# Kernel optimization log

Measured on AMD Instinct MI355X. Metric: run time of the kernel, lower is better.

The kernel has to match this reference:

```python
import jax, jax.numpy as jnp
import numpy as np

H = 1024      # hidden_size
M = 64        # matrix_dim = int(sqrt(4096))
R = 2         # rank
LS = 2048     # local_size = budget_size // 2


def setup_inputs() -> dict:
    key = jax.random.key(0)
    ks = jax.random.split(key, 12)
    B, S = 4, 2048
    def lin(k, fan_in, fan_out):
        # stored as [in, out] so forward is x @ W
        return jax.random.normal(k, (fan_in, fan_out), dtype=jnp.float32) / np.sqrt(fan_in)
    return {
        "x": jax.random.normal(ks[0], (B, S, H), dtype=jnp.float32),
        "W_decay": lin(ks[1], H, 1),
        "W_key": lin(ks[2], H, R * M),
        "W_value": lin(ks[3], H, R * M),
        "W_ql": lin(ks[4], H, M),
        "W_qr": lin(ks[5], H, M),
        "W_rec_out": lin(ks[6], M, H),
        "W_up": lin(ks[7], H, LS),
        "W_gate": lin(ks[8], H, LS),
        "W_down": lin(ks[9], LS, H),
        "init_state": jnp.zeros((M, M), dtype=jnp.float32),
    }


def reference(x, W_decay, W_key, W_value, W_ql, W_qr, W_rec_out, W_up, W_gate, W_down, init_state):
    B, S, _ = x.shape
    # Precompute all per-token projections (vectorized over batch & seq)
    decay = jax.nn.sigmoid(x @ W_decay)[..., 0]            # [B,S]
    keys = (x @ W_key).reshape(B, S, R, M)                 # [B,S,R,M]
    values = (x @ W_value).reshape(B, S, R, M)             # [B,S,R,M]
    write = jnp.einsum('bsrm,bsrn->bsmn', keys, values) / float(R)  # [B,S,M,M]
    ql = x @ W_ql                                          # [B,S,M]
    qr = x @ W_qr                                          # [B,S,M]

    def step(state, inp):
        d, w, ql_t, qr_t = inp                             # d:[B], w:[B,M,M], ql/qr:[B,M]
        d3 = d[:, None, None]
        state = d3 * state + (1.0 - d3) * w                # decayed matrix-state update
        read = jnp.einsum('bm,bmn->bn', ql_t, state) * qr_t  # [B,M]
        return state, read

    state0 = jnp.broadcast_to(init_state, (B, M, M))
    # scan over time axis (time-major inputs)
    _, reads = jax.lax.scan(
        step, state0,
        (decay.transpose(1, 0), write.transpose(1, 0, 2, 3),
         ql.transpose(1, 0, 2), qr.transpose(1, 0, 2)))
    reads = reads.transpose(1, 0, 2)                       # [B,S,M]

    recurrent = jax.nn.silu(reads) @ W_rec_out             # [B,S,H]
    local = ((x @ W_up) * jax.nn.silu(x @ W_gate)) @ W_down  # SwiGLU branch
    return recurrent + local
```

## Files before the change

kernel.cpp:

```cpp
#include <hip/hip_runtime.h>
#include <hip/hip_bf16.h>

typedef __bf16 bf16x8 __attribute__((ext_vector_type(8)));
typedef float f32x4 __attribute__((ext_vector_type(4)));

#define BS   8192
#define Hd   1024
#define LSd  2048
#define Md   64

static __device__ __forceinline__ float bfu2f(unsigned short u) {
  return __uint_as_float(((unsigned int)u) << 16);
}
static __device__ __forceinline__ __hip_bfloat16 f2bf(float f) { return __float2bfloat16(f); }


__global__ __launch_bounds__(256) void conv_bf16_kernel(const float* __restrict__ src,
    __hip_bfloat16* __restrict__ dst, int n) {
  int i = (blockIdx.x * 256 + threadIdx.x) * 4;
  if (i + 3 < n) {
    float4 f = *(const float4*)(src + i);
    dst[i + 0] = f2bf(f.x); dst[i + 1] = f2bf(f.y);
    dst[i + 2] = f2bf(f.z); dst[i + 3] = f2bf(f.w);
  }
}

__global__ __launch_bounds__(256) void prep_wcat_kernel(const float* __restrict__ Wd,
    const float* __restrict__ Wk, const float* __restrict__ Wv,
    const float* __restrict__ Wql, const float* __restrict__ Wqr,
    __hip_bfloat16* __restrict__ out) {
  int i = blockIdx.x * 256 + threadIdx.x;
  int n = i >> 10, h = i & 1023;
  float v = 0.f;
  if (n == 0)        v = Wd[h];
  else if (n < 129)  v = Wk[h * 128 + (n - 1)];
  else if (n < 257)  v = Wv[h * 128 + (n - 129)];
  else if (n < 321)  v = Wql[h * 64 + (n - 257)];
  else if (n < 385)  v = Wqr[h * 64 + (n - 321)];
  out[i] = f2bf(v);
}

__global__ __launch_bounds__(256) void transpose_conv_kernel(const float* __restrict__ src,
    __hip_bfloat16* __restrict__ dst, int R, int C, int c_off) {
  __shared__ float tile[32][33];
  int bc = blockIdx.x * 32, br = blockIdx.y * 32;
  int tx = threadIdx.x & 31, ty = threadIdx.x >> 5;
  #pragma unroll
  for (int i = 0; i < 32; i += 8)
    tile[ty + i][tx] = src[(size_t)(br + ty + i) * C + bc + tx];
  __syncthreads();
  #pragma unroll
  for (int i = 0; i < 32; i += 8)
    dst[(size_t)(bc + c_off + ty + i) * R + br + tx] = f2bf(tile[tx][ty + i]);
}


static __device__ __forceinline__ void stage_tile(const __hip_bfloat16* __restrict__ src, int ld,
    __hip_bfloat16* __restrict__ dst, int tid) {
  #pragma unroll
  for (int it = 0; it < 2; ++it) {
    int idx = tid + it * 256;
    int r = idx >> 2, cc = (idx & 3) * 8;
    *(uint4*)(dst + r * 32 + cc) = *(const uint4*)(src + (size_t)r * ld + cc);
  }
}

static __device__ __forceinline__ void mfma_tiles(const __hip_bfloat16* sA, const __hip_bfloat16* sB,
    int wm, int wn, int fr, int qk, f32x4 acc[4][4]) {
  bf16x8 af[4], bg[4];
  #pragma unroll
  for (int i = 0; i < 4; ++i) af[i] = *(const bf16x8*)(sA + (wm + i * 16 + fr) * 32 + qk);
  #pragma unroll
  for (int j = 0; j < 4; ++j) bg[j] = *(const bf16x8*)(sB + (wn + j * 16 + fr) * 32 + qk);
  #pragma unroll
  for (int i = 0; i < 4; ++i)
    #pragma unroll
    for (int j = 0; j < 4; ++j)
      acc[i][j] = __builtin_amdgcn_mfma_f32_16x16x32_bf16(af[i], bg[j], acc[i][j], 0, 0, 0);
}

__global__ __launch_bounds__(256, 2) void gemm_proj_kernel(const __hip_bfloat16* __restrict__ A,
    const __hip_bfloat16* __restrict__ Bt, float* __restrict__ C) {
  __shared__ __align__(16) __hip_bfloat16 sA[128 * 32];
  __shared__ __align__(16) __hip_bfloat16 sB[128 * 32];
  int tid = threadIdx.x, nb = blockIdx.x, mb = blockIdx.y;
  int wave = tid >> 6, lane = tid & 63;
  int wm = (wave >> 1) * 64, wn = (wave & 1) * 64;
  int fr = lane & 15, qk = (lane >> 4) * 8, q4 = (lane >> 4) * 4;
  f32x4 acc[4][4] = {};
  const __hip_bfloat16* Atile = A + (size_t)mb * 128 * Hd;
  const __hip_bfloat16* Btile = Bt + (size_t)nb * 128 * Hd;
  for (int kt = 0; kt < Hd; kt += 32) {
    __syncthreads();
    stage_tile(Atile + kt, Hd, sA, tid);
    stage_tile(Btile + kt, Hd, sB, tid);
    __syncthreads();
    mfma_tiles(sA, sB, wm, wn, fr, qk, acc);
  }
  #pragma unroll
  for (int i = 0; i < 4; ++i)
    #pragma unroll
    for (int j = 0; j < 4; ++j) {
      int row = mb * 128 + wm + i * 16 + q4;
      int col = nb * 128 + wn + j * 16 + fr;
      #pragma unroll
      for (int rg = 0; rg < 4; ++rg)
        C[(size_t)(row + rg) * 512 + col] = acc[i][j][rg];
    }
}

__global__ __launch_bounds__(256, 2) void gemm_upgate_kernel(const __hip_bfloat16* __restrict__ A,
    const __hip_bfloat16* __restrict__ Bt, __hip_bfloat16* __restrict__ hout) {
  __shared__ __align__(16) __hip_bfloat16 sA[128 * 32];
  __shared__ __align__(16) __hip_bfloat16 sBu[128 * 32];
  __shared__ __align__(16) __hip_bfloat16 sBg[128 * 32];
  int tid = threadIdx.x, nb = blockIdx.x, mb = blockIdx.y;
  int wave = tid >> 6, lane = tid & 63;
  int wm = (wave >> 1) * 64, wn = (wave & 1) * 64;
  int fr = lane & 15, qk = (lane >> 4) * 8, q4 = (lane >> 4) * 4;
  f32x4 accu[4][4] = {}, accg[4][4] = {};
  const __hip_bfloat16* Atile = A + (size_t)mb * 128 * Hd;
  const __hip_bfloat16* Bu = Bt + (size_t)(nb * 128) * Hd;
  const __hip_bfloat16* Bg = Bt + (size_t)(2048 + nb * 128) * Hd;
  for (int kt = 0; kt < Hd; kt += 32) {
    __syncthreads();
    stage_tile(Atile + kt, Hd, sA, tid);
    stage_tile(Bu + kt, Hd, sBu, tid);
    stage_tile(Bg + kt, Hd, sBg, tid);
    __syncthreads();
    mfma_tiles(sA, sBu, wm, wn, fr, qk, accu);
    mfma_tiles(sA, sBg, wm, wn, fr, qk, accg);
  }
  #pragma unroll
  for (int i = 0; i < 4; ++i)
    #pragma unroll
    for (int j = 0; j < 4; ++j) {
      int col = nb * 128 + wn + j * 16 + fr;
      #pragma unroll
      for (int rg = 0; rg < 4; ++rg) {
        int row = mb * 128 + wm + i * 16 + q4 + rg;
        float u = accu[i][j][rg], g = accg[i][j][rg];
        float hv = u * g / (1.f + __expf(-g));
        hout[(size_t)row * LSd + col] = f2bf(hv);
      }
    }
}

__global__ __launch_bounds__(256, 2) void gemm_final_kernel(const __hip_bfloat16* __restrict__ A,
    const __hip_bfloat16* __restrict__ Bt, const __hip_bfloat16* __restrict__ A2,
    const __hip_bfloat16* __restrict__ B2t, float* __restrict__ C) {
  __shared__ __align__(16) __hip_bfloat16 sA[128 * 32];
  __shared__ __align__(16) __hip_bfloat16 sB[128 * 32];
  int tid = threadIdx.x, nb = blockIdx.x, mb = blockIdx.y;
  int wave = tid >> 6, lane = tid & 63;
  int wm = (wave >> 1) * 64, wn = (wave & 1) * 64;
  int fr = lane & 15, qk = (lane >> 4) * 8, q4 = (lane >> 4) * 4;
  f32x4 acc[4][4] = {};
  const __hip_bfloat16* Atile = A + (size_t)mb * 128 * LSd;
  const __hip_bfloat16* Btile = Bt + (size_t)nb * 128 * LSd;
  for (int kt = 0; kt < LSd; kt += 32) {
    __syncthreads();
    stage_tile(Atile + kt, LSd, sA, tid);
    stage_tile(Btile + kt, LSd, sB, tid);
    __syncthreads();
    mfma_tiles(sA, sB, wm, wn, fr, qk, acc);
  }
  const __hip_bfloat16* A2t = A2 + (size_t)mb * 128 * Md;
  const __hip_bfloat16* B2tile = B2t + (size_t)nb * 128 * Md;
  for (int kt = 0; kt < Md; kt += 32) {
    __syncthreads();
    stage_tile(A2t + kt, Md, sA, tid);
    stage_tile(B2tile + kt, Md, sB, tid);
    __syncthreads();
    mfma_tiles(sA, sB, wm, wn, fr, qk, acc);
  }
  #pragma unroll
  for (int i = 0; i < 4; ++i)
    #pragma unroll
    for (int j = 0; j < 4; ++j) {
      int row = mb * 128 + wm + i * 16 + q4;
      int col = nb * 128 + wn + j * 16 + fr;
      #pragma unroll
      for (int rg = 0; rg < 4; ++rg)
        C[(size_t)(row + rg) * Hd + col] = acc[i][j][rg];
    }
}


__global__ __launch_bounds__(256) void scan_chunk_kernel(const float* __restrict__ proj,
    float* __restrict__ Lam, float* __restrict__ udv, float* __restrict__ alpha,
    float* __restrict__ dS) {
  int bc = blockIdx.x, t0 = bc * 64, tid = threadIdx.x;
  __shared__ float d_s[64], ld_s[64], Lam_s[64], u_s[64];
  __shared__ __align__(16) __hip_bfloat16 k_s[128 * 64];
  __shared__ __align__(16) __hip_bfloat16 v_s[128 * 64];
  if (tid < 64) {
    float z = proj[(size_t)(t0 + tid) * 512];
    float dd = 1.f / (1.f + __expf(-z));
    float l = (z >= 0.f) ? -log1pf(__expf(-z)) : (z - log1pf(__expf(z)));
    d_s[tid] = dd; ld_s[tid] = l;
  }
  __syncthreads();
  if (tid == 0) {
    float s = 0.f;
    for (int j = 0; j < 64; ++j) { s += ld_s[j]; Lam_s[j] = s; }
  }
  __syncthreads();
  float Lend = Lam_s[63];
  if (tid < 64) {
    u_s[tid] = (1.f - d_s[tid]) * __expf(Lend - Lam_s[tid]) * 0.5f;
    Lam[t0 + tid] = Lam_s[tid];
    udv[t0 + tid] = (1.f - d_s[tid]) * 0.5f;
  }
  if (tid == 0) alpha[bc] = __expf(Lend);
  __syncthreads();
  for (int i = tid; i < 128 * 64; i += 256) {
    int jr = i >> 6, m = i & 63, j = jr >> 1, r = jr & 1;
    const float* rowp = proj + (size_t)(t0 + j) * 512;
    k_s[i] = f2bf(u_s[j] * rowp[1 + r * 64 + m]);
    v_s[i] = f2bf(rowp[129 + r * 64 + m]);
  }
  __syncthreads();
  int m0 = (tid & 15) * 4, n0 = (tid >> 4) * 4;
  float acc[4][4] = {{0.f}};
  for (int jr = 0; jr < 128; ++jr) {
    ushort4 ku = *(const ushort4*)&k_s[jr * 64 + m0];
    ushort4 vu = *(const ushort4*)&v_s[jr * 64 + n0];
    float k0 = bfu2f(ku.x), k1 = bfu2f(ku.y), k2 = bfu2f(ku.z), k3 = bfu2f(ku.w);
    float v0 = bfu2f(vu.x), v1 = bfu2f(vu.y), v2 = bfu2f(vu.z), v3 = bfu2f(vu.w);
    acc[0][0] += k0 * v0; acc[0][1] += k0 * v1; acc[0][2] += k0 * v2; acc[0][3] += k0 * v3;
    acc[1][0] += k1 * v0; acc[1][1] += k1 * v1; acc[1][2] += k1 * v2; acc[1][3] += k1 * v3;
    acc[2][0] += k2 * v0; acc[2][1] += k2 * v1; acc[2][2] += k2 * v2; acc[2][3] += k2 * v3;
    acc[3][0] += k3 * v0; acc[3][1] += k3 * v1; acc[3][2] += k3 * v2; acc[3][3] += k3 * v3;
  }
  float* outp = dS + (size_t)bc * 4096;
  #pragma unroll
  for (int a = 0; a < 4; ++a)
    #pragma unroll
    for (int b2 = 0; b2 < 4; ++b2)
      outp[(m0 + a) * 64 + (n0 + b2)] = acc[a][b2];
}

__global__ __launch_bounds__(256) void scan_cross_kernel(const float* __restrict__ dS,
    const float* __restrict__ alpha, const float* __restrict__ init_state,
    float* __restrict__ Sin) {
  int idx = blockIdx.x * 256 + threadIdx.x;
  int b = idx >> 12, e = idx & 4095;
  float s = init_state[e];
  for (int c = 0; c < 32; ++c) {
    int bc = b * 32 + c;
    Sin[(size_t)bc * 4096 + e] = s;
    s = alpha[bc] * s + dS[(size_t)bc * 4096 + e];
  }
}

#define QLD 68

__global__ __launch_bounds__(256) void scan_read_kernel(const float* __restrict__ proj,
    const float* __restrict__ Lam, const float* __restrict__ udv,
    const float* __restrict__ Sin, __hip_bfloat16* __restrict__ Rd) {
  int bc = blockIdx.x, t0 = bc * 64, tid = threadIdx.x;
  __shared__ __align__(16) __hip_bfloat16 ql_s[64 * QLD];
  __shared__ __align__(16) __hip_bfloat16 kv_s[128 * 64];
  __shared__ __align__(16) __hip_bfloat16 S_s[64 * 64];
  __shared__ __align__(16) __hip_bfloat16 P_s[128 * 64];
  __shared__ float Lam_s[64], ud_s[64], eL_s[64];
  for (int i = tid; i < 64 * 64; i += 256) {
    int t = i >> 6, m = i & 63;
    ql_s[t * QLD + m] = f2bf(proj[(size_t)(t0 + t) * 512 + 257 + m]);
    S_s[i] = f2bf(Sin[(size_t)bc * 4096 + i]);
  }
  for (int i = tid; i < 128 * 64; i += 256) {
    int jr = i >> 6, m = i & 63, j = jr >> 1, r = jr & 1;
    kv_s[i] = f2bf(proj[(size_t)(t0 + j) * 512 + 1 + r * 64 + m]);
  }
  if (tid < 64) {
    float L = Lam[t0 + tid];
    Lam_s[tid] = L; ud_s[tid] = udv[t0 + tid]; eL_s[tid] = __expf(L);
  }
  __syncthreads();
  int tr = (tid & 15) * 4, n0 = (tid >> 4) * 4;
  float acc[4][4] = {{0.f}};
  for (int mb4 = 0; mb4 < 64; mb4 += 4) {
    float sm[4][4];
    #pragma unroll
    for (int mm = 0; mm < 4; ++mm) {
      ushort4 sv = *(const ushort4*)&S_s[(mb4 + mm) * 64 + n0];
      sm[mm][0] = bfu2f(sv.x); sm[mm][1] = bfu2f(sv.y);
      sm[mm][2] = bfu2f(sv.z); sm[mm][3] = bfu2f(sv.w);
    }
    #pragma unroll
    for (int a = 0; a < 4; ++a) {
      ushort4 qa = *(const ushort4*)&ql_s[(tr + a) * QLD + mb4];
      float q0 = bfu2f(qa.x), q1 = bfu2f(qa.y), q2 = bfu2f(qa.z), q3 = bfu2f(qa.w);
      #pragma unroll
      for (int b2 = 0; b2 < 4; ++b2)
        acc[a][b2] += q0 * sm[0][b2] + q1 * sm[1][b2] + q2 * sm[2][b2] + q3 * sm[3][b2];
    }
  }
  #pragma unroll
  for (int a = 0; a < 4; ++a) {
    float e = eL_s[tr + a];
    #pragma unroll
    for (int b2 = 0; b2 < 4; ++b2) acc[a][b2] *= e;
  }
  {
    int jr = tid >> 1, j = jr >> 1, tb = (tid & 1) * 32;
    float dot[32];
    #pragma unroll
    for (int t2 = 0; t2 < 32; ++t2) dot[t2] = 0.f;
    for (int m = 0; m < 64; m += 4) {
      ushort4 kb = *(const ushort4*)&kv_s[jr * 64 + m];
      float k0 = bfu2f(kb.x), k1 = bfu2f(kb.y), k2 = bfu2f(kb.z), k3 = bfu2f(kb.w);
      #pragma unroll
      for (int t2 = 0; t2 < 32; ++t2) {
        ushort4 qa = *(const ushort4*)&ql_s[(tb + t2) * QLD + m];
        dot[t2] += bfu2f(qa.x) * k0 + bfu2f(qa.y) * k1 + bfu2f(qa.z) * k2 + bfu2f(qa.w) * k3;
      }
    }
    #pragma unroll
    for (int t2 = 0; t2 < 32; ++t2) {
      int t = tb + t2;
      float coef = (j <= t) ? ud_s[j] * __expf(Lam_s[t] - Lam_s[j]) : 0.f;
      P_s[jr * 64 + t] = f2bf(dot[t2] * coef);
    }
  }
  __syncthreads();
  for (int i = tid; i < 128 * 64; i += 256) {
    int jr = i >> 6, m = i & 63, j = jr >> 1, r = jr & 1;
    kv_s[i] = f2bf(proj[(size_t)(t0 + j) * 512 + 129 + r * 64 + m]);
  }
  __syncthreads();
  for (int jr = 0; jr < 128; ++jr) {
    ushort4 pu = *(const ushort4*)&P_s[jr * 64 + tr];
    ushort4 vu = *(const ushort4*)&kv_s[jr * 64 + n0];
    float p0 = bfu2f(pu.x), p1 = bfu2f(pu.y), p2 = bfu2f(pu.z), p3 = bfu2f(pu.w);
    float v0 = bfu2f(vu.x), v1 = bfu2f(vu.y), v2 = bfu2f(vu.z), v3 = bfu2f(vu.w);
    acc[0][0] += p0 * v0; acc[0][1] += p0 * v1; acc[0][2] += p0 * v2; acc[0][3] += p0 * v3;
    acc[1][0] += p1 * v0; acc[1][1] += p1 * v1; acc[1][2] += p1 * v2; acc[1][3] += p1 * v3;
    acc[2][0] += p2 * v0; acc[2][1] += p2 * v1; acc[2][2] += p2 * v2; acc[2][3] += p2 * v3;
    acc[3][0] += p3 * v0; acc[3][1] += p3 * v1; acc[3][2] += p3 * v2; acc[3][3] += p3 * v3;
  }
  #pragma unroll
  for (int a = 0; a < 4; ++a) {
    int t = t0 + tr + a;
    const float* qrp = proj + (size_t)t * 512 + 321;
    #pragma unroll
    for (int b2 = 0; b2 < 4; ++b2) {
      float rv = acc[a][b2] * qrp[n0 + b2];
      float sv = rv / (1.f + __expf(-rv));
      Rd[(size_t)t * 64 + n0 + b2] = f2bf(sv);
    }
  }
}


extern "C" void kernel_launch(void* const* d_in, const int* in_sizes, int n_in,
                              void* d_out, int out_size, void* d_ws, size_t ws_size,
                              hipStream_t stream) {
  const float* x      = (const float*)d_in[0];
  const float* W_dec  = (const float*)d_in[1];
  const float* W_key  = (const float*)d_in[2];
  const float* W_val  = (const float*)d_in[3];
  const float* W_ql   = (const float*)d_in[4];
  const float* W_qr   = (const float*)d_in[5];
  const float* W_rec  = (const float*)d_in[6];
  const float* W_up   = (const float*)d_in[7];
  const float* W_gate = (const float*)d_in[8];
  const float* W_down = (const float*)d_in[9];
  const float* init_state = (const float*)d_in[10];
  float* out = (float*)d_out;

  char* w = (char*)d_ws;
  auto take = [&](size_t bytes) { char* p = w; w += (bytes + 255) & ~(size_t)255; return p; };
  __hip_bfloat16* x_bf   = (__hip_bfloat16*)take((size_t)BS * Hd * 2);
  __hip_bfloat16* Wcat_t = (__hip_bfloat16*)take((size_t)512 * Hd * 2);
  __hip_bfloat16* Wug_t  = (__hip_bfloat16*)take((size_t)4096 * Hd * 2);
  __hip_bfloat16* Wdn_t  = (__hip_bfloat16*)take((size_t)Hd * LSd * 2);
  __hip_bfloat16* Wrc_t  = (__hip_bfloat16*)take((size_t)Hd * Md * 2);
  float* proj  = (float*)take((size_t)BS * 512 * 4);
  float* Lam   = (float*)take((size_t)BS * 4);
  float* udv   = (float*)take((size_t)BS * 4);
  float* alpha = (float*)take((size_t)128 * 4);
  float* dS    = (float*)take((size_t)128 * 4096 * 4);
  float* Sin   = (float*)take((size_t)128 * 4096 * 4);
  __hip_bfloat16* Rd   = (__hip_bfloat16*)take((size_t)BS * Md * 2);
  __hip_bfloat16* hbuf = (__hip_bfloat16*)take((size_t)BS * LSd * 2);

  conv_bf16_kernel<<<8192, 256, 0, stream>>>(x, x_bf, BS * Hd);
  prep_wcat_kernel<<<2048, 256, 0, stream>>>(W_dec, W_key, W_val, W_ql, W_qr, Wcat_t);
  transpose_conv_kernel<<<dim3(64, 32), 256, 0, stream>>>(W_up,   Wug_t, Hd, LSd, 0);
  transpose_conv_kernel<<<dim3(64, 32), 256, 0, stream>>>(W_gate, Wug_t, Hd, LSd, 2048);
  transpose_conv_kernel<<<dim3(32, 64), 256, 0, stream>>>(W_down, Wdn_t, LSd, Hd, 0);
  transpose_conv_kernel<<<dim3(32, 2),  256, 0, stream>>>(W_rec,  Wrc_t, Md, Hd, 0);

  gemm_proj_kernel<<<dim3(4, 64), 256, 0, stream>>>(x_bf, Wcat_t, proj);

  scan_chunk_kernel<<<128, 256, 0, stream>>>(proj, Lam, udv, alpha, dS);
  scan_cross_kernel<<<64, 256, 0, stream>>>(dS, alpha, init_state, Sin);
  scan_read_kernel<<<128, 256, 0, stream>>>(proj, Lam, udv, Sin, Rd);

  gemm_upgate_kernel<<<dim3(16, 64), 256, 0, stream>>>(x_bf, Wug_t, hbuf);
  gemm_final_kernel<<<dim3(8, 64), 256, 0, stream>>>(hbuf, Wdn_t, Rd, Wrc_t, out);
}
```

Measured before the change: 338.6 us.

## Stage GEMM tiles with direct global-to-LDS loads in fragment-major layout

```diff
diff --git a/kernel.cpp b/kernel.cpp
--- a/kernel.cpp
+++ b/kernel.cpp
@@ -20,8 +20,12 @@
   int i = (blockIdx.x * 256 + threadIdx.x) * 4;
   if (i + 3 < n) {
     float4 f = *(const float4*)(src + i);
-    dst[i + 0] = f2bf(f.x); dst[i + 1] = f2bf(f.y);
-    dst[i + 2] = f2bf(f.z); dst[i + 3] = f2bf(f.w);
+    ushort4 o;
+    o.x = (unsigned short)(__bfloat16_as_ushort(f2bf(f.x)));
+    o.y = (unsigned short)(__bfloat16_as_ushort(f2bf(f.y)));
+    o.z = (unsigned short)(__bfloat16_as_ushort(f2bf(f.z)));
+    o.w = (unsigned short)(__bfloat16_as_ushort(f2bf(f.w)));
+    *(ushort4*)(dst + i) = o;
   }
 }
 
@@ -55,28 +59,51 @@
 }
 
 
-static __device__ __forceinline__ void stage_tile(const __hip_bfloat16* __restrict__ src, int ld,
-    __hip_bfloat16* __restrict__ dst, int tid) {
+static __device__ __forceinline__ void stage_async(const __hip_bfloat16* __restrict__ src, int ld,
+    __hip_bfloat16* __restrict__ dst, int wave, int lane) {
+  int fr = lane & 15, ch = lane >> 4;
   #pragma unroll
   for (int it = 0; it < 2; ++it) {
-    int idx = tid + it * 256;
-    int r = idx >> 2, cc = (idx & 3) * 8;
-    *(uint4*)(dst + r * 32 + cc) = *(const uint4*)(src + (size_t)r * ld + cc);
-  }
-}
-
-static __device__ __forceinline__ void mfma_tiles(const __hip_bfloat16* sA, const __hip_bfloat16* sB,
-    int wm, int wn, int fr, int qk, f32x4 acc[4][4]) {
+    int ri = wave * 2 + it;
+    int row = ri * 16 + fr;
+    __builtin_amdgcn_global_load_lds(
+        (const __attribute__((address_space(1))) void*)(src + (size_t)row * ld + ch * 8),
+        (__attribute__((address_space(3))) void*)(dst + ri * 512),
+        16, 0, 0);
+  }
+}
+
+static __device__ __forceinline__ void mfma_single(const __hip_bfloat16* sA, const __hip_bfloat16* sB,
+    int wm16, int wn16, int lane, f32x4 acc[4][4]) {
   bf16x8 af[4], bg[4];
   #pragma unroll
-  for (int i = 0; i < 4; ++i) af[i] = *(const bf16x8*)(sA + (wm + i * 16 + fr) * 32 + qk);
-  #pragma unroll
-  for (int j = 0; j < 4; ++j) bg[j] = *(const bf16x8*)(sB + (wn + j * 16 + fr) * 32 + qk);
+  for (int i = 0; i < 4; ++i) af[i] = *(const bf16x8*)(sA + (wm16 + i) * 512 + lane * 8);
+  #pragma unroll
+  for (int j = 0; j < 4; ++j) bg[j] = *(const bf16x8*)(sB + (wn16 + j) * 512 + lane * 8);
   #pragma unroll
   for (int i = 0; i < 4; ++i)
     #pragma unroll
     for (int j = 0; j < 4; ++j)
       acc[i][j] = __builtin_amdgcn_mfma_f32_16x16x32_bf16(af[i], bg[j], acc[i][j], 0, 0, 0);
+}
+
+static __device__ __forceinline__ void mfma_dual(const __hip_bfloat16* sA,
+    const __hip_bfloat16* sBu, const __hip_bfloat16* sBg,
+    int wm16, int wn16, int lane, f32x4 accu[4][4], f32x4 accg[4][4]) {
+  bf16x8 af[4], bu[4], bg[4];
+  #pragma unroll
+  for (int i = 0; i < 4; ++i) af[i] = *(const bf16x8*)(sA + (wm16 + i) * 512 + lane * 8);
+  #pragma unroll
+  for (int j = 0; j < 4; ++j) bu[j] = *(const bf16x8*)(sBu + (wn16 + j) * 512 + lane * 8);
+  #pragma unroll
+  for (int j = 0; j < 4; ++j) bg[j] = *(const bf16x8*)(sBg + (wn16 + j) * 512 + lane * 8);
+  #pragma unroll
+  for (int i = 0; i < 4; ++i)
+    #pragma unroll
+    for (int j = 0; j < 4; ++j) {
+      accu[i][j] = __builtin_amdgcn_mfma_f32_16x16x32_bf16(af[i], bu[j], accu[i][j], 0, 0, 0);
+      accg[i][j] = __builtin_amdgcn_mfma_f32_16x16x32_bf16(af[i], bg[j], accg[i][j], 0, 0, 0);
+    }
 }
 
 __global__ __launch_bounds__(256, 2) void gemm_proj_kernel(const __hip_bfloat16* __restrict__ A,
@@ -85,24 +112,24 @@
   __shared__ __align__(16) __hip_bfloat16 sB[128 * 32];
   int tid = threadIdx.x, nb = blockIdx.x, mb = blockIdx.y;
   int wave = tid >> 6, lane = tid & 63;
-  int wm = (wave >> 1) * 64, wn = (wave & 1) * 64;
-  int fr = lane & 15, qk = (lane >> 4) * 8, q4 = (lane >> 4) * 4;
+  int wm16 = (wave >> 1) * 4, wn16 = (wave & 1) * 4;
+  int fr = lane & 15, q4 = (lane >> 4) * 4;
   f32x4 acc[4][4] = {};
   const __hip_bfloat16* Atile = A + (size_t)mb * 128 * Hd;
   const __hip_bfloat16* Btile = Bt + (size_t)nb * 128 * Hd;
   for (int kt = 0; kt < Hd; kt += 32) {
     __syncthreads();
-    stage_tile(Atile + kt, Hd, sA, tid);
-    stage_tile(Btile + kt, Hd, sB, tid);
-    __syncthreads();
-    mfma_tiles(sA, sB, wm, wn, fr, qk, acc);
+    stage_async(Atile + kt, Hd, sA, wave, lane);
+    stage_async(Btile + kt, Hd, sB, wave, lane);
+    __syncthreads();
+    mfma_single(sA, sB, wm16, wn16, lane, acc);
   }
   #pragma unroll
   for (int i = 0; i < 4; ++i)
     #pragma unroll
     for (int j = 0; j < 4; ++j) {
-      int row = mb * 128 + wm + i * 16 + q4;
-      int col = nb * 128 + wn + j * 16 + fr;
+      int row = mb * 128 + (wm16 + i) * 16 + q4;
+      int col = nb * 128 + (wn16 + j) * 16 + fr;
       #pragma unroll
       for (int rg = 0; rg < 4; ++rg)
         C[(size_t)(row + rg) * 512 + col] = acc[i][j][rg];
@@ -116,29 +143,28 @@
   __shared__ __align__(16) __hip_bfloat16 sBg[128 * 32];
   int tid = threadIdx.x, nb = blockIdx.x, mb = blockIdx.y;
   int wave = tid >> 6, lane = tid & 63;
-  int wm = (wave >> 1) * 64, wn = (wave & 1) * 64;
-  int fr = lane & 15, qk = (lane >> 4) * 8, q4 = (lane >> 4) * 4;
+  int wm16 = (wave >> 1) * 4, wn16 = (wave & 1) * 4;
+  int fr = lane & 15, q4 = (lane >> 4) * 4;
   f32x4 accu[4][4] = {}, accg[4][4] = {};
   const __hip_bfloat16* Atile = A + (size_t)mb * 128 * Hd;
   const __hip_bfloat16* Bu = Bt + (size_t)(nb * 128) * Hd;
   const __hip_bfloat16* Bg = Bt + (size_t)(2048 + nb * 128) * Hd;
   for (int kt = 0; kt < Hd; kt += 32) {
     __syncthreads();
-    stage_tile(Atile + kt, Hd, sA, tid);
-    stage_tile(Bu + kt, Hd, sBu, tid);
-    stage_tile(Bg + kt, Hd, sBg, tid);
-    __syncthreads();
-    mfma_tiles(sA, sBu, wm, wn, fr, qk, accu);
-    mfma_tiles(sA, sBg, wm, wn, fr, qk, accg);
+    stage_async(Atile + kt, Hd, sA, wave, lane);
+    stage_async(Bu + kt, Hd, sBu, wave, lane);
+    stage_async(Bg + kt, Hd, sBg, wave, lane);
+    __syncthreads();
+    mfma_dual(sA, sBu, sBg, wm16, wn16, lane, accu, accg);
   }
   #pragma unroll
   for (int i = 0; i < 4; ++i)
     #pragma unroll
     for (int j = 0; j < 4; ++j) {
-      int col = nb * 128 + wn + j * 16 + fr;
+      int col = nb * 128 + (wn16 + j) * 16 + fr;
       #pragma unroll
       for (int rg = 0; rg < 4; ++rg) {
-        int row = mb * 128 + wm + i * 16 + q4 + rg;
+        int row = mb * 128 + (wm16 + i) * 16 + q4 + rg;
         float u = accu[i][j][rg], g = accg[i][j][rg];
         float hv = u * g / (1.f + __expf(-g));
         hout[(size_t)row * LSd + col] = f2bf(hv);
@@ -153,33 +179,33 @@
   __shared__ __align__(16) __hip_bfloat16 sB[128 * 32];
   int tid = threadIdx.x, nb = blockIdx.x, mb = blockIdx.y;
   int wave = tid >> 6, lane = tid & 63;
-  int wm = (wave >> 1) * 64, wn = (wave & 1) * 64;
-  int fr = lane & 15, qk = (lane >> 4) * 8, q4 = (lane >> 4) * 4;
+  int wm16 = (wave >> 1) * 4, wn16 = (wave & 1) * 4;
+  int fr = lane & 15, q4 = (lane >> 4) * 4;
   f32x4 acc[4][4] = {};
   const __hip_bfloat16* Atile = A + (size_t)mb * 128 * LSd;
   const __hip_bfloat16* Btile = Bt + (size_t)nb * 128 * LSd;
   for (int kt = 0; kt < LSd; kt += 32) {
     __syncthreads();
-    stage_tile(Atile + kt, LSd, sA, tid);
-    stage_tile(Btile + kt, LSd, sB, tid);
-    __syncthreads();
-    mfma_tiles(sA, sB, wm, wn, fr, qk, acc);
+    stage_async(Atile + kt, LSd, sA, wave, lane);
+    stage_async(Btile + kt, LSd, sB, wave, lane);
+    __syncthreads();
+    mfma_single(sA, sB, wm16, wn16, lane, acc);
   }
   const __hip_bfloat16* A2t = A2 + (size_t)mb * 128 * Md;
   const __hip_bfloat16* B2tile = B2t + (size_t)nb * 128 * Md;
   for (int kt = 0; kt < Md; kt += 32) {
     __syncthreads();
-    stage_tile(A2t + kt, Md, sA, tid);
-    stage_tile(B2tile + kt, Md, sB, tid);
-    __syncthreads();
-    mfma_tiles(sA, sB, wm, wn, fr, qk, acc);
+    stage_async(A2t + kt, Md, sA, wave, lane);
+    stage_async(B2tile + kt, Md, sB, wave, lane);
+    __syncthreads();
+    mfma_single(sA, sB, wm16, wn16, lane, acc);
   }
   #pragma unroll
   for (int i = 0; i < 4; ++i)
     #pragma unroll
     for (int j = 0; j < 4; ++j) {
-      int row = mb * 128 + wm + i * 16 + q4;
-      int col = nb * 128 + wn + j * 16 + fr;
+      int row = mb * 128 + (wm16 + i) * 16 + q4;
+      int col = nb * 128 + (wn16 + j) * 16 + fr;
       #pragma unroll
       for (int rg = 0; rg < 4; ++rg)
         C[(size_t)(row + rg) * Hd + col] = acc[i][j][rg];
```

Result: slower. 379.1 us (+12.0%).
